# Kernel tuning notes

Hardware: AMD Instinct MI355X
Metric: run time of the kernel (lower is better)

The kernel has to match this reference:

```python
import jax, jax.numpy as jnp
import numpy as np

NUM_LAYERS = 3
CODEBOOK_SIZE = 2048
EMBED_DIM = 256
B, T = 16, 2048


def setup_inputs() -> dict:
    key = jax.random.key(0)
    k1, k2 = jax.random.split(key)
    h = jax.random.normal(k1, (B, T, EMBED_DIM), dtype=jnp.float32)
    codebooks = jax.random.normal(k2, (NUM_LAYERS, CODEBOOK_SIZE, EMBED_DIM), dtype=jnp.float32)
    return {"h": h, "codebooks": codebooks}


def reference(h, codebooks):
    """Residual VQ: 3 sequential layers of nearest-codeword quantization.
    h: (B, T, D); codebooks: (L, K, D).
    Returns (quantized_total (B,T,D), indices (L, B, T)).
    """
    residual = h
    quantized_total = jnp.zeros_like(h)
    all_indices = []
    for l in range(codebooks.shape[0]):
        W = codebooks[l]  # (K, D)
        # ||r - w||^2 = ||r||^2 - 2 r.w + ||w||^2 ; same argmin as the naive broadcast form.
        r_sq = jnp.sum(residual * residual, axis=-1, keepdims=True)         # (B, T, 1)
        w_sq = jnp.sum(W * W, axis=-1)                                      # (K,)
        cross = jnp.einsum('btd,kd->btk', residual, W)                      # (B, T, K)
        dists = r_sq - 2.0 * cross + w_sq                                   # (B, T, K)
        indices = jnp.argmin(dists, axis=-1)                                # (B, T)
        all_indices.append(indices)
        quant = W[indices]                                                  # gather -> (B, T, D)
        quantized_total = quantized_total + quant
        residual = residual - quant
    return quantized_total, jnp.stack(all_indices, axis=0)
```

## Files before the change

kernel.cpp:

```cpp
#include <hip/hip_runtime.h>
#include <math.h>

#define NUM_LAYERS 3
#define KCB 2048
#define DIM 256
#define NROWS 32768
#define NQ (NROWS * DIM)

#define F_BYTES (3u * 128u * 16384u)

#define BSH_OFF  0
#define BV_OFF   131072
#define BI_OFF   132096
#define BIDX_OFF 133120
#define SMEM_BYTES 133632

typedef _Float16 half8 __attribute__((ext_vector_type(8)));
typedef float   f32x4 __attribute__((ext_vector_type(4)));

__global__ void rvq_wsq(const float* __restrict__ cb, float* __restrict__ wsq)
{
    int tid = blockIdx.x * 256 + threadIdx.x;
    const float* p = cb + (size_t)tid * DIM;
    float s = 0.f;
    #pragma unroll
    for (int u = 0; u < 64; ++u) {
        float4 v = *(const float4*)(p + u * 4);
        s = fmaf(v.x, v.x, s); s = fmaf(v.y, v.y, s);
        s = fmaf(v.z, v.z, s); s = fmaf(v.w, v.w, s);
    }
    wsq[tid] = s;
}

__global__ void rvq_repack(const float* __restrict__ cb, unsigned short* __restrict__ F)
{
    int b = blockIdx.x;
    int layer = b >> 10;
    int rem   = b & 1023;
    int tn    = rem >> 3;
    int kb    = rem & 7;
    int lane  = threadIdx.x;

    int cw = tn * 16 + (lane & 15);
    int k0 = kb * 32 + (lane >> 4) * 8;
    const float* src = cb + ((size_t)(layer * KCB + cw)) * DIM + k0;
    float4 x0 = *(const float4*)(src);
    float4 x1 = *(const float4*)(src + 4);
    float v[8] = {x0.x, x0.y, x0.z, x0.w, x1.x, x1.y, x1.z, x1.w};

    half8 hi, lo;
    #pragma unroll
    for (int j = 0; j < 8; ++j) {
        _Float16 h = (_Float16)v[j];
        hi[j] = h;
        lo[j] = (_Float16)(v[j] - (float)h);
    }
    size_t base = ((size_t)b) * 1024;
    *(half8*)(F + base + lane * 8)        = hi;
    *(half8*)(F + base + 512 + lane * 8)  = lo;
}

__device__ __forceinline__ void stage_chunk(const char* Fb, char* Bsh,
                                            int c, int buf, int wv, int lane)
{
    #pragma unroll
    for (int i = 0; i < 8; ++i) {
        int s = wv * 8 + i;
        int tm = s >> 5;
        int off = (s & 31) * 1024;
        const char* g = Fb + (size_t)tm * 1048576 + (size_t)c * 32768 + off + (size_t)lane * 16;
        char* lp = Bsh + (size_t)buf * 65536 + (size_t)tm * 32768 + off + (size_t)lane * 16;
        __builtin_amdgcn_global_load_lds(
            (const __attribute__((address_space(1))) unsigned int*)g,
            (__attribute__((address_space(3))) unsigned int*)lp, 16, 0, 0);
    }
}

__global__ __launch_bounds__(512, 2)
void rvq_main(const float* __restrict__ h,
              const float* __restrict__ cb,
              const unsigned short* __restrict__ F,
              const float* __restrict__ wsq,
              float* __restrict__ out)
{
    extern __shared__ char smem[];
    char*  Bsh     = smem + BSH_OFF;
    float* bV_sh   = (float*)(smem + BV_OFF);
    int*   bI_sh   = (int*)  (smem + BI_OFF);
    int*   bidx_sh = (int*)  (smem + BIDX_OFF);

    const int t      = threadIdx.x;
    const int lane   = t & 63;
    const int wv     = t >> 6;
    const int team   = wv & 1;
    const int rgroup = wv >> 1;
    const int rowB   = blockIdx.x * 128;
    const int row0w  = rowB + rgroup * 32;
    const int arow   = lane & 15;
    const int aq     = lane >> 4;

    half8 ahi[2][8], alo[2][8];
    float s2[2];
    #pragma unroll
    for (int mi = 0; mi < 2; ++mi) {
        s2[mi] = 0.f;
        #pragma unroll
        for (int kb = 0; kb < 8; ++kb) {
            const float* p = h + (size_t)(row0w + mi * 16 + arow) * DIM + kb * 32 + aq * 8;
            float4 x0 = *(const float4*)(p);
            float4 x1 = *(const float4*)(p + 4);
            float v[8] = {x0.x, x0.y, x0.z, x0.w, x1.x, x1.y, x1.z, x1.w};
            #pragma unroll
            for (int j = 0; j < 8; ++j) {
                _Float16 hv = (_Float16)v[j];
                ahi[mi][kb][j] = hv;
                alo[mi][kb][j] = (_Float16)(v[j] - (float)hv);
                s2[mi] = fmaf(v[j], v[j], s2[mi]);
            }
        }
    }

    stage_chunk((const char*)F, Bsh, 0, 0, wv, lane);

    for (int l = 0; l < NUM_LAYERS; ++l) {
        const float* __restrict__ Wl  = cb + (size_t)l * KCB * DIM;
        const float* __restrict__ wql = wsq + l * KCB;
        const char*  Fb = (const char*)F + (size_t)l * 2097152;

        float a0 = s2[0], a1 = s2[1];
        a0 += __shfl_xor(a0, 16); a0 += __shfl_xor(a0, 32);
        a1 += __shfl_xor(a1, 16); a1 += __shfl_xor(a1, 32);
        float rsqC[2][4];
        #pragma unroll
        for (int i = 0; i < 4; ++i) {
            rsqC[0][i] = __shfl(a0, aq * 4 + i, 16);
            rsqC[1][i] = __shfl(a1, aq * 4 + i, 16);
        }

        float bestV[2][4];
        int   bestI[2][4];
        #pragma unroll
        for (int mi = 0; mi < 2; ++mi)
            #pragma unroll
            for (int i = 0; i < 4; ++i) { bestV[mi][i] = INFINITY; bestI[mi][i] = 0; }

        __syncthreads();

        for (int c = 0; c < 32; ++c) {
            const int cur = c & 1;
            if (c + 1 < 32) stage_chunk(Fb, Bsh, c + 1, 1 - cur, wv, lane);

            #pragma unroll
            for (int ti = 0; ti < 2; ++ti) {
                const char* base = Bsh + (size_t)cur * 65536 + (size_t)team * 32768 + (size_t)ti * 16384;
                f32x4 acc[2][2];
                const f32x4 z = {0.f, 0.f, 0.f, 0.f};
                acc[0][0] = z; acc[0][1] = z; acc[1][0] = z; acc[1][1] = z;
                #pragma unroll
                for (int kb = 0; kb < 8; ++kb) {
                    half8 bhi = *(const half8*)(base + kb * 2048 + lane * 16);
                    half8 blo = *(const half8*)(base + kb * 2048 + 1024 + lane * 16);
                    const int p = kb & 1;
                    acc[0][p] = __builtin_amdgcn_mfma_f32_16x16x32_f16(ahi[0][kb], bhi, acc[0][p], 0, 0, 0);
                    acc[1][p] = __builtin_amdgcn_mfma_f32_16x16x32_f16(ahi[1][kb], bhi, acc[1][p], 0, 0, 0);
                    acc[0][p] = __builtin_amdgcn_mfma_f32_16x16x32_f16(alo[0][kb], bhi, acc[0][p], 0, 0, 0);
                    acc[1][p] = __builtin_amdgcn_mfma_f32_16x16x32_f16(alo[1][kb], bhi, acc[1][p], 0, 0, 0);
                    acc[0][p] = __builtin_amdgcn_mfma_f32_16x16x32_f16(ahi[0][kb], blo, acc[0][p], 0, 0, 0);
                    acc[1][p] = __builtin_amdgcn_mfma_f32_16x16x32_f16(ahi[1][kb], blo, acc[1][p], 0, 0, 0);
                }
                const int col = team * 1024 + (c * 2 + ti) * 16 + arow;
                const float wq = wql[col];
                #pragma unroll
                for (int mi = 0; mi < 2; ++mi)
                    #pragma unroll
                    for (int i = 0; i < 4; ++i) {
                        float cc = acc[mi][0][i] + acc[mi][1][i];
                        float dist = (rsqC[mi][i] - 2.f * cc) + wq;
                        if (dist < bestV[mi][i]) { bestV[mi][i] = dist; bestI[mi][i] = col; }
                    }
            }
            __syncthreads();
        }

        #pragma unroll
        for (int mi = 0; mi < 2; ++mi)
            #pragma unroll
            for (int i = 0; i < 4; ++i) {
                float bv = bestV[mi][i]; int bi = bestI[mi][i];
                #pragma unroll
                for (int s = 8; s; s >>= 1) {
                    float ov = __shfl_xor(bv, s, 16);
                    int   oi = __shfl_xor(bi, s, 16);
                    if (ov < bv || (ov == bv && oi < bi)) { bv = ov; bi = oi; }
                }
                bestV[mi][i] = bv; bestI[mi][i] = bi;
            }
        if (arow == 0) {
            #pragma unroll
            for (int mi = 0; mi < 2; ++mi)
                #pragma unroll
                for (int i = 0; i < 4; ++i) {
                    bV_sh[wv * 32 + mi * 16 + aq * 4 + i] = bestV[mi][i];
                    bI_sh[wv * 32 + mi * 16 + aq * 4 + i] = bestI[mi][i];
                }
        }
        __syncthreads();

        if (t < 128) {
            int rg = t >> 5, rl = t & 31;
            float v0 = bV_sh[(rg * 2 + 0) * 32 + rl]; int i0 = bI_sh[(rg * 2 + 0) * 32 + rl];
            float v1 = bV_sh[(rg * 2 + 1) * 32 + rl]; int i1 = bI_sh[(rg * 2 + 1) * 32 + rl];
            int bi = (v1 < v0 || (v1 == v0 && i1 < i0)) ? i1 : i0;
            bidx_sh[t] = bi;
            out[NQ + (size_t)l * NROWS + rowB + t] = (float)bi;
        }
        if (l < NUM_LAYERS - 1)
            stage_chunk(Fb + 2097152, Bsh, 0, 0, wv, lane);
        __syncthreads();

        if (l < NUM_LAYERS - 1) {
            #pragma unroll
            for (int mi = 0; mi < 2; ++mi) {
                const int bi = bidx_sh[rgroup * 32 + mi * 16 + arow];
                const float* wrow = Wl + (size_t)bi * DIM;
                float ns = 0.f;
                #pragma unroll
                for (int kb = 0; kb < 8; ++kb) {
                    const float* wp = wrow + kb * 32 + aq * 8;
                    float4 w0 = *(const float4*)(wp);
                    float4 w1 = *(const float4*)(wp + 4);
                    float wv8[8] = {w0.x, w0.y, w0.z, w0.w, w1.x, w1.y, w1.z, w1.w};
                    #pragma unroll
                    for (int j = 0; j < 8; ++j) {
                        float r = ((float)ahi[mi][kb][j] + (float)alo[mi][kb][j]) - wv8[j];
                        _Float16 hv = (_Float16)r;
                        ahi[mi][kb][j] = hv;
                        alo[mi][kb][j] = (_Float16)(r - (float)hv);
                        ns = fmaf(r, r, ns);
                    }
                }
                s2[mi] = ns;
            }
        } else {
            const int mi  = team;
            const int row = row0w + mi * 16 + arow;
            const int bi  = bidx_sh[rgroup * 32 + mi * 16 + arow];
            const float* wrow = Wl + (size_t)bi * DIM;
            #pragma unroll
            for (int kb = 0; kb < 8; ++kb) {
                const float* wp = wrow + kb * 32 + aq * 8;
                const float* hp = h + (size_t)row * DIM + kb * 32 + aq * 8;
                float4 w0 = *(const float4*)(wp);
                float4 w1 = *(const float4*)(wp + 4);
                float4 h0 = *(const float4*)(hp);
                float4 h1 = *(const float4*)(hp + 4);
                float wv8[8] = {w0.x, w0.y, w0.z, w0.w, w1.x, w1.y, w1.z, w1.w};
                float hv8[8] = {h0.x, h0.y, h0.z, h0.w, h1.x, h1.y, h1.z, h1.w};
                float o[8];
                #pragma unroll
                for (int j = 0; j < 8; ++j) {
                    float r = ((float)ahi[mi][kb][j] + (float)alo[mi][kb][j]) - wv8[j];
                    o[j] = hv8[j] - r;
                }
                float* op = out + (size_t)row * DIM + kb * 32 + aq * 8;
                *(float4*)(op)     = make_float4(o[0], o[1], o[2], o[3]);
                *(float4*)(op + 4) = make_float4(o[4], o[5], o[6], o[7]);
            }
        }
    }
}

extern "C" void kernel_launch(void* const* d_in, const int* in_sizes, int n_in,
                              void* d_out, int out_size, void* d_ws, size_t ws_size,
                              hipStream_t stream) {
    const float* h  = (const float*)d_in[0];
    const float* cb = (const float*)d_in[1];
    float* out = (float*)d_out;
    unsigned short* F = (unsigned short*)d_ws;
    float* wsq = (float*)((char*)d_ws + F_BYTES);

    hipFuncSetAttribute((const void*)rvq_main,
                        hipFuncAttributeMaxDynamicSharedMemorySize, SMEM_BYTES);

    rvq_wsq   <<<dim3(24),   dim3(256), 0, stream>>>(cb, wsq);
    rvq_repack<<<dim3(3072), dim3(64),  0, stream>>>(cb, F);
    rvq_main  <<<dim3(NROWS / 128), dim3(512), SMEM_BYTES, stream>>>(h, cb, F, wsq, out);
}
```

Baseline: 413.4 us.

## Switch distance GEMM from 16x16x32 to 32x32x16 MFMA tiles

Each wave now computes one 32-row by 32-codeword tile with the 32x32x16 f16 MFMA, replacing two 16x16 tiles per row half. The codebook repack layout, A-operand register layout, residual-norm distribution (now staged through shared memory), argmin reduction and epilogue indexing are all reorganized to match the new fragment layout. The larger tile is meant to raise MFMA efficiency and reduce LDS B-fragment reads per FLOP. The cost is 16-entry accumulators and best-value arrays, which raise register pressure and may hurt occupancy.

Result: slower. 473.8 us (+14.6%).

```diff
diff --git a/kernel.cpp b/kernel.cpp
--- a/kernel.cpp
+++ b/kernel.cpp
@@ -7,16 +7,17 @@
 #define NROWS 32768
 #define NQ (NROWS * DIM)
 
-#define F_BYTES (3u * 128u * 16384u)
+#define F_BYTES (3u * 2097152u)
 
 #define BSH_OFF  0
-#define BV_OFF   131072
-#define BI_OFF   132096
-#define BIDX_OFF 133120
-#define SMEM_BYTES 133632
+#define RSQ_OFF  131072
+#define BV_OFF   131584
+#define BI_OFF   132608
+#define BIDX_OFF 133632
+#define SMEM_BYTES 134144
 
 typedef _Float16 half8 __attribute__((ext_vector_type(8)));
-typedef float   f32x4 __attribute__((ext_vector_type(4)));
+typedef float   f32x16 __attribute__((ext_vector_type(16)));
 
 __global__ void rvq_wsq(const float* __restrict__ cb, float* __restrict__ wsq)
 {
@@ -37,12 +38,13 @@
     int b = blockIdx.x;
     int layer = b >> 10;
     int rem   = b & 1023;
-    int tn    = rem >> 3;
-    int kb    = rem & 7;
+    int team  = rem >> 9;
+    int c     = (rem >> 4) & 31;
+    int ks    = rem & 15;
     int lane  = threadIdx.x;
 
-    int cw = tn * 16 + (lane & 15);
-    int k0 = kb * 32 + (lane >> 4) * 8;
+    int cw = team * 1024 + c * 32 + (lane & 31);
+    int k0 = ks * 16 + (lane >> 5) * 8;
     const float* src = cb + ((size_t)(layer * KCB + cw)) * DIM + k0;
     float4 x0 = *(const float4*)(src);
     float4 x1 = *(const float4*)(src + 4);
@@ -85,6 +87,7 @@
 {
     extern __shared__ char smem[];
     char*  Bsh     = smem + BSH_OFF;
+    float* rsq_sh  = (float*)(smem + RSQ_OFF);
     float* bV_sh   = (float*)(smem + BV_OFF);
     int*   bI_sh   = (int*)  (smem + BI_OFF);
     int*   bidx_sh = (int*)  (smem + BIDX_OFF);
@@ -96,26 +99,24 @@
     const int rgroup = wv >> 1;
     const int rowB   = blockIdx.x * 128;
     const int row0w  = rowB + rgroup * 32;
-    const int arow   = lane & 15;
-    const int aq     = lane >> 4;
-
-    half8 ahi[2][8], alo[2][8];
-    float s2[2];
-    #pragma unroll
-    for (int mi = 0; mi < 2; ++mi) {
-        s2[mi] = 0.f;
-        #pragma unroll
-        for (int kb = 0; kb < 8; ++kb) {
-            const float* p = h + (size_t)(row0w + mi * 16 + arow) * DIM + kb * 32 + aq * 8;
-            float4 x0 = *(const float4*)(p);
-            float4 x1 = *(const float4*)(p + 4);
+    const int ln     = lane & 31;
+    const int lh     = lane >> 5;
+
+    half8 ahi[16], alo[16];
+    float s2 = 0.f;
+    {
+        const float* rp = h + (size_t)(row0w + ln) * DIM + lh * 8;
+        #pragma unroll
+        for (int ks = 0; ks < 16; ++ks) {
+            float4 x0 = *(const float4*)(rp + ks * 16);
+            float4 x1 = *(const float4*)(rp + ks * 16 + 4);
             float v[8] = {x0.x, x0.y, x0.z, x0.w, x1.x, x1.y, x1.z, x1.w};
             #pragma unroll
             for (int j = 0; j < 8; ++j) {
                 _Float16 hv = (_Float16)v[j];
-                ahi[mi][kb][j] = hv;
-                alo[mi][kb][j] = (_Float16)(v[j] - (float)hv);
-                s2[mi] = fmaf(v[j], v[j], s2[mi]);
+                ahi[ks][j] = hv;
+                alo[ks][j] = (_Float16)(v[j] - (float)hv);
+                s2 = fmaf(v[j], v[j], s2);
             }
         }
     }
@@ -127,82 +128,69 @@
         const float* __restrict__ wql = wsq + l * KCB;
         const char*  Fb = (const char*)F + (size_t)l * 2097152;
 
-        float a0 = s2[0], a1 = s2[1];
-        a0 += __shfl_xor(a0, 16); a0 += __shfl_xor(a0, 32);
-        a1 += __shfl_xor(a1, 16); a1 += __shfl_xor(a1, 32);
-        float rsqC[2][4];
-        #pragma unroll
-        for (int i = 0; i < 4; ++i) {
-            rsqC[0][i] = __shfl(a0, aq * 4 + i, 16);
-            rsqC[1][i] = __shfl(a1, aq * 4 + i, 16);
-        }
-
-        float bestV[2][4];
-        int   bestI[2][4];
-        #pragma unroll
-        for (int mi = 0; mi < 2; ++mi)
-            #pragma unroll
-            for (int i = 0; i < 4; ++i) { bestV[mi][i] = INFINITY; bestI[mi][i] = 0; }
-
+        float rs = s2 + __shfl_xor(s2, 32);
+        if (team == 0 && lh == 0) rsq_sh[rgroup * 32 + ln] = rs;
         __syncthreads();
+
+        float rsqR[16];
+        #pragma unroll
+        for (int r = 0; r < 16; ++r)
+            rsqR[r] = rsq_sh[rgroup * 32 + (r & 3) + 8 * (r >> 2) + 4 * lh];
+
+        float bestV[16];
+        int   bestI[16];
+        #pragma unroll
+        for (int r = 0; r < 16; ++r) { bestV[r] = INFINITY; bestI[r] = 0; }
 
         for (int c = 0; c < 32; ++c) {
             const int cur = c & 1;
             if (c + 1 < 32) stage_chunk(Fb, Bsh, c + 1, 1 - cur, wv, lane);
 
-            #pragma unroll
-            for (int ti = 0; ti < 2; ++ti) {
-                const char* base = Bsh + (size_t)cur * 65536 + (size_t)team * 32768 + (size_t)ti * 16384;
-                f32x4 acc[2][2];
-                const f32x4 z = {0.f, 0.f, 0.f, 0.f};
-                acc[0][0] = z; acc[0][1] = z; acc[1][0] = z; acc[1][1] = z;
-                #pragma unroll
-                for (int kb = 0; kb < 8; ++kb) {
-                    half8 bhi = *(const half8*)(base + kb * 2048 + lane * 16);
-                    half8 blo = *(const half8*)(base + kb * 2048 + 1024 + lane * 16);
-                    const int p = kb & 1;
-                    acc[0][p] = __builtin_amdgcn_mfma_f32_16x16x32_f16(ahi[0][kb], bhi, acc[0][p], 0, 0, 0);
-                    acc[1][p] = __builtin_amdgcn_mfma_f32_16x16x32_f16(ahi[1][kb], bhi, acc[1][p], 0, 0, 0);
-                    acc[0][p] = __builtin_amdgcn_mfma_f32_16x16x32_f16(alo[0][kb], bhi, acc[0][p], 0, 0, 0);
-                    acc[1][p] = __builtin_amdgcn_mfma_f32_16x16x32_f16(alo[1][kb], bhi, acc[1][p], 0, 0, 0);
-                    acc[0][p] = __builtin_amdgcn_mfma_f32_16x16x32_f16(ahi[0][kb], blo, acc[0][p], 0, 0, 0);
-                    acc[1][p] = __builtin_amdgcn_mfma_f32_16x16x32_f16(ahi[1][kb], blo, acc[1][p], 0, 0, 0);
+            const char* base = Bsh + (size_t)cur * 65536 + (size_t)team * 32768;
+            f32x16 acc0 = {}, acc1 = {};
+            #pragma unroll
+            for (int ks = 0; ks < 16; ++ks) {
+                half8 bhi = *(const half8*)(base + ks * 2048 + lane * 16);
+                half8 blo = *(const half8*)(base + ks * 2048 + 1024 + lane * 16);
+                if (ks & 1) {
+                    acc1 = __builtin_amdgcn_mfma_f32_32x32x16_f16(ahi[ks], bhi, acc1, 0, 0, 0);
+                    acc1 = __builtin_amdgcn_mfma_f32_32x32x16_f16(alo[ks], bhi, acc1, 0, 0, 0);
+                    acc1 = __builtin_amdgcn_mfma_f32_32x32x16_f16(ahi[ks], blo, acc1, 0, 0, 0);
+                } else {
+                    acc0 = __builtin_amdgcn_mfma_f32_32x32x16_f16(ahi[ks], bhi, acc0, 0, 0, 0);
+                    acc0 = __builtin_amdgcn_mfma_f32_32x32x16_f16(alo[ks], bhi, acc0, 0, 0, 0);
+                    acc0 = __builtin_amdgcn_mfma_f32_32x32x16_f16(ahi[ks], blo, acc0, 0, 0, 0);
                 }
-                const int col = team * 1024 + (c * 2 + ti) * 16 + arow;
-                const float wq = wql[col];
-                #pragma unroll
-                for (int mi = 0; mi < 2; ++mi)
-                    #pragma unroll
-                    for (int i = 0; i < 4; ++i) {
-                        float cc = acc[mi][0][i] + acc[mi][1][i];
-                        float dist = (rsqC[mi][i] - 2.f * cc) + wq;
-                        if (dist < bestV[mi][i]) { bestV[mi][i] = dist; bestI[mi][i] = col; }
-                    }
+            }
+            const int col = team * 1024 + c * 32 + ln;
+            const float wq = wql[col];
+            #pragma unroll
+            for (int r = 0; r < 16; ++r) {
+                float cc = acc0[r] + acc1[r];
+                float dist = (rsqR[r] - 2.f * cc) + wq;
+                if (dist < bestV[r]) { bestV[r] = dist; bestI[r] = col; }
             }
             __syncthreads();
         }
 
         #pragma unroll
-        for (int mi = 0; mi < 2; ++mi)
-            #pragma unroll
-            for (int i = 0; i < 4; ++i) {
-                float bv = bestV[mi][i]; int bi = bestI[mi][i];
-                #pragma unroll
-                for (int s = 8; s; s >>= 1) {
-                    float ov = __shfl_xor(bv, s, 16);
-                    int   oi = __shfl_xor(bi, s, 16);
-                    if (ov < bv || (ov == bv && oi < bi)) { bv = ov; bi = oi; }
-                }
-                bestV[mi][i] = bv; bestI[mi][i] = bi;
-            }
-        if (arow == 0) {
-            #pragma unroll
-            for (int mi = 0; mi < 2; ++mi)
-                #pragma unroll
-                for (int i = 0; i < 4; ++i) {
-                    bV_sh[wv * 32 + mi * 16 + aq * 4 + i] = bestV[mi][i];
-                    bI_sh[wv * 32 + mi * 16 + aq * 4 + i] = bestI[mi][i];
-                }
+        for (int r = 0; r < 16; ++r) {
+            float bv = bestV[r]; int bi = bestI[r];
+            #pragma unroll
+            for (int s = 16; s; s >>= 1) {
+                float ov = __shfl_xor(bv, s);
+                int   oi = __shfl_xor(bi, s);
+                if (ov < bv || (ov == bv && oi < bi)) { bv = ov; bi = oi; }
+            }
+            bestV[r] = bv; bestI[r] = bi;
+        }
+        if (ln == 0) {
+            #pragma unroll
+            for (int r = 0; r < 16; ++r) {
+                int row = (r & 3) + 8 * (r >> 2) + 4 * lh;
+                bV_sh[wv * 32 + row] = bestV[r];
+                bI_sh[wv * 32 + row] = bestI[r];
+            }
         }
         __syncthreads();
 
@@ -219,52 +207,47 @@
         __syncthreads();
 
         if (l < NUM_LAYERS - 1) {
-            #pragma unroll
-            for (int mi = 0; mi < 2; ++mi) {
-                const int bi = bidx_sh[rgroup * 32 + mi * 16 + arow];
-                const float* wrow = Wl + (size_t)bi * DIM;
-                float ns = 0.f;
+            const int bi = bidx_sh[rgroup * 32 + ln];
+            const float* wrow = Wl + (size_t)bi * DIM + lh * 8;
+            float ns = 0.f;
+            #pragma unroll
+            for (int ks = 0; ks < 16; ++ks) {
+                float4 w0 = *(const float4*)(wrow + ks * 16);
+                float4 w1 = *(const float4*)(wrow + ks * 16 + 4);
+                float wv8[8] = {w0.x, w0.y, w0.z, w0.w, w1.x, w1.y, w1.z, w1.w};
                 #pragma unroll
-                for (int kb = 0; kb < 8; ++kb) {
-                    const float* wp = wrow + kb * 32 + aq * 8;
-                    float4 w0 = *(const float4*)(wp);
-                    float4 w1 = *(const float4*)(wp + 4);
-                    float wv8[8] = {w0.x, w0.y, w0.z, w0.w, w1.x, w1.y, w1.z, w1.w};
-                    #pragma unroll
-                    for (int j = 0; j < 8; ++j) {
-                        float r = ((float)ahi[mi][kb][j] + (float)alo[mi][kb][j]) - wv8[j];
-                        _Float16 hv = (_Float16)r;
-                        ahi[mi][kb][j] = hv;
-                        alo[mi][kb][j] = (_Float16)(r - (float)hv);
-                        ns = fmaf(r, r, ns);
-                    }
+                for (int j = 0; j < 8; ++j) {
+                    float r = ((float)ahi[ks][j] + (float)alo[ks][j]) - wv8[j];
+                    _Float16 hv = (_Float16)r;
+                    ahi[ks][j] = hv;
+                    alo[ks][j] = (_Float16)(r - (float)hv);
+                    ns = fmaf(r, r, ns);
                 }
-                s2[mi] = ns;
-            }
+            }
+            s2 = ns;
         } else {
-            const int mi  = team;
-            const int row = row0w + mi * 16 + arow;
-            const int bi  = bidx_sh[rgroup * 32 + mi * 16 + arow];
-            const float* wrow = Wl + (size_t)bi * DIM;
-            #pragma unroll
-            for (int kb = 0; kb < 8; ++kb) {
-                const float* wp = wrow + kb * 32 + aq * 8;
-                const float* hp = h + (size_t)row * DIM + kb * 32 + aq * 8;
-                float4 w0 = *(const float4*)(wp);
-                float4 w1 = *(const float4*)(wp + 4);
-                float4 h0 = *(const float4*)(hp);
-                float4 h1 = *(const float4*)(hp + 4);
+            const int row = row0w + ln;
+            const int bi  = bidx_sh[rgroup * 32 + ln];
+            const float* wrow = Wl + (size_t)bi * DIM + lh * 8;
+            const float* hp   = h + (size_t)row * DIM + lh * 8;
+            float* op         = out + (size_t)row * DIM + lh * 8;
+            #pragma unroll
+            for (int ksi = 0; ksi < 8; ++ksi) {
+                const int ks = team * 8 + ksi;
+                float4 w0 = *(const float4*)(wrow + ks * 16);
+                float4 w1 = *(const float4*)(wrow + ks * 16 + 4);
+                float4 h0 = *(const float4*)(hp + ks * 16);
+                float4 h1 = *(const float4*)(hp + ks * 16 + 4);
                 float wv8[8] = {w0.x, w0.y, w0.z, w0.w, w1.x, w1.y, w1.z, w1.w};
                 float hv8[8] = {h0.x, h0.y, h0.z, h0.w, h1.x, h1.y, h1.z, h1.w};
                 float o[8];
                 #pragma unroll
                 for (int j = 0; j < 8; ++j) {
-                    float r = ((float)ahi[mi][kb][j] + (float)alo[mi][kb][j]) - wv8[j];
+                    float r = ((float)ahi[ks][j] + (float)alo[ks][j]) - wv8[j];
                     o[j] = hv8[j] - r;
                 }
-                float* op = out + (size_t)row * DIM + kb * 32 + aq * 8;
-                *(float4*)(op)     = make_float4(o[0], o[1], o[2], o[3]);
-                *(float4*)(op + 4) = make_float4(o[4], o[5], o[6], o[7]);
+                *(float4*)(op + ks * 16)     = make_float4(o[0], o[1], o[2], o[3]);
+                *(float4*)(op + ks * 16 + 4) = make_float4(o[4], o[5], o[6], o[7]);
             }
         }
     }
```

## Split the K dimension across wave pairs and exchange partial dot products via LDS

Applied to the files above, without the earlier changes.

Each wave pair now splits the 256-wide reduction dimension in half instead of splitting codewords. Each wave keeps only half of the A fragments in registers, which halves per-thread fp16 register storage. Both waves compute partials for two 16-codeword tiles and swap one partial through a new LDS exchange buffer. Staging chunks shrink to 32 codewords with a 64-iteration loop, and LDS use drops from about 133 KB to about 102 KB. In exchange it adds LDS traffic and a partial-sum exchange per chunk, with a barrier on every iteration.

Result: faster. 374.5 us (-9.4%).

```diff
diff --git a/kernel.cpp b/kernel.cpp
--- a/kernel.cpp
+++ b/kernel.cpp
@@ -10,10 +10,12 @@
 #define F_BYTES (3u * 128u * 16384u)
 
 #define BSH_OFF  0
-#define BV_OFF   131072
-#define BI_OFF   132096
-#define BIDX_OFF 133120
-#define SMEM_BYTES 133632
+#define XCH_OFF  65536
+#define RSQP_OFF 98304
+#define BV_OFF   99328
+#define BI_OFF   100352
+#define BIDX_OFF 101376
+#define SMEM_BYTES 101888
 
 typedef _Float16 half8 __attribute__((ext_vector_type(8)));
 typedef float   f32x4 __attribute__((ext_vector_type(4)));
@@ -60,20 +62,47 @@
     *(half8*)(F + base + 512 + lane * 8)  = lo;
 }
 
-__device__ __forceinline__ void stage_chunk(const char* Fb, char* Bsh,
-                                            int c, int buf, int wv, int lane)
-{
-    #pragma unroll
-    for (int i = 0; i < 8; ++i) {
-        int s = wv * 8 + i;
-        int tm = s >> 5;
-        int off = (s & 31) * 1024;
-        const char* g = Fb + (size_t)tm * 1048576 + (size_t)c * 32768 + off + (size_t)lane * 16;
-        char* lp = Bsh + (size_t)buf * 65536 + (size_t)tm * 32768 + off + (size_t)lane * 16;
+__device__ __forceinline__ void stage_chunk32(const char* Fb, char* dst, int c, int t)
+{
+    const char* g = Fb + (size_t)c * 32768;
+    #pragma unroll
+    for (int i = 0; i < 4; ++i) {
+        int off = (i * 512 + t) * 16;
         __builtin_amdgcn_global_load_lds(
-            (const __attribute__((address_space(1))) unsigned int*)g,
-            (__attribute__((address_space(3))) unsigned int*)lp, 16, 0, 0);
-    }
+            (const __attribute__((address_space(1))) unsigned int*)(g + off),
+            (__attribute__((address_space(3))) unsigned int*)(dst + off), 16, 0, 0);
+    }
+}
+
+__device__ __forceinline__ void tile_partial(
+    const char* tbase, const half8 (&ahi)[2][4], const half8 (&alo)[2][4],
+    int kt, int lane, f32x4 (&po)[2])
+{
+    const f32x4 z = {0.f, 0.f, 0.f, 0.f};
+    f32x4 a00 = z, a01 = z, a10 = z, a11 = z;
+    #pragma unroll
+    for (int kq = 0; kq < 4; ++kq) {
+        const int kb = kt * 4 + kq;
+        half8 bhi = *(const half8*)(tbase + kb * 2048 + lane * 16);
+        half8 blo = *(const half8*)(tbase + kb * 2048 + 1024 + lane * 16);
+        if (kq & 1) {
+            a01 = __builtin_amdgcn_mfma_f32_16x16x32_f16(ahi[0][kq], bhi, a01, 0, 0, 0);
+            a11 = __builtin_amdgcn_mfma_f32_16x16x32_f16(ahi[1][kq], bhi, a11, 0, 0, 0);
+            a01 = __builtin_amdgcn_mfma_f32_16x16x32_f16(alo[0][kq], bhi, a01, 0, 0, 0);
+            a11 = __builtin_amdgcn_mfma_f32_16x16x32_f16(alo[1][kq], bhi, a11, 0, 0, 0);
+            a01 = __builtin_amdgcn_mfma_f32_16x16x32_f16(ahi[0][kq], blo, a01, 0, 0, 0);
+            a11 = __builtin_amdgcn_mfma_f32_16x16x32_f16(ahi[1][kq], blo, a11, 0, 0, 0);
+        } else {
+            a00 = __builtin_amdgcn_mfma_f32_16x16x32_f16(ahi[0][kq], bhi, a00, 0, 0, 0);
+            a10 = __builtin_amdgcn_mfma_f32_16x16x32_f16(ahi[1][kq], bhi, a10, 0, 0, 0);
+            a00 = __builtin_amdgcn_mfma_f32_16x16x32_f16(alo[0][kq], bhi, a00, 0, 0, 0);
+            a10 = __builtin_amdgcn_mfma_f32_16x16x32_f16(alo[1][kq], bhi, a10, 0, 0, 0);
+            a00 = __builtin_amdgcn_mfma_f32_16x16x32_f16(ahi[0][kq], blo, a00, 0, 0, 0);
+            a10 = __builtin_amdgcn_mfma_f32_16x16x32_f16(ahi[1][kq], blo, a10, 0, 0, 0);
+        }
+    }
+    #pragma unroll
+    for (int i = 0; i < 4; ++i) { po[0][i] = a00[i] + a01[i]; po[1][i] = a10[i] + a11[i]; }
 }
 
 __global__ __launch_bounds__(512, 2)
@@ -85,42 +114,44 @@
 {
     extern __shared__ char smem[];
     char*  Bsh     = smem + BSH_OFF;
+    char*  Xch     = smem + XCH_OFF;
+    float* rsqp    = (float*)(smem + RSQP_OFF);
     float* bV_sh   = (float*)(smem + BV_OFF);
     int*   bI_sh   = (int*)  (smem + BI_OFF);
     int*   bidx_sh = (int*)  (smem + BIDX_OFF);
 
-    const int t      = threadIdx.x;
-    const int lane   = t & 63;
-    const int wv     = t >> 6;
-    const int team   = wv & 1;
-    const int rgroup = wv >> 1;
-    const int rowB   = blockIdx.x * 128;
-    const int row0w  = rowB + rgroup * 32;
-    const int arow   = lane & 15;
-    const int aq     = lane >> 4;
-
-    half8 ahi[2][8], alo[2][8];
+    const int t     = threadIdx.x;
+    const int lane  = t & 63;
+    const int wv    = t >> 6;
+    const int kt    = wv & 1;
+    const int rg    = wv >> 1;
+    const int rowB  = blockIdx.x * 128;
+    const int row0w = rowB + rg * 32;
+    const int arow  = lane & 15;
+    const int aq    = lane >> 4;
+
+    half8 ahi[2][4], alo[2][4];
     float s2[2];
     #pragma unroll
     for (int mi = 0; mi < 2; ++mi) {
         s2[mi] = 0.f;
         #pragma unroll
-        for (int kb = 0; kb < 8; ++kb) {
-            const float* p = h + (size_t)(row0w + mi * 16 + arow) * DIM + kb * 32 + aq * 8;
+        for (int kq = 0; kq < 4; ++kq) {
+            const float* p = h + (size_t)(row0w + mi * 16 + arow) * DIM + (kt * 4 + kq) * 32 + aq * 8;
             float4 x0 = *(const float4*)(p);
             float4 x1 = *(const float4*)(p + 4);
             float v[8] = {x0.x, x0.y, x0.z, x0.w, x1.x, x1.y, x1.z, x1.w};
             #pragma unroll
             for (int j = 0; j < 8; ++j) {
                 _Float16 hv = (_Float16)v[j];
-                ahi[mi][kb][j] = hv;
-                alo[mi][kb][j] = (_Float16)(v[j] - (float)hv);
+                ahi[mi][kq][j] = hv;
+                alo[mi][kq][j] = (_Float16)(v[j] - (float)hv);
                 s2[mi] = fmaf(v[j], v[j], s2[mi]);
             }
         }
     }
 
-    stage_chunk((const char*)F, Bsh, 0, 0, wv, lane);
+    stage_chunk32((const char*)F, Bsh, 0, t);
 
     for (int l = 0; l < NUM_LAYERS; ++l) {
         const float* __restrict__ Wl  = cb + (size_t)l * KCB * DIM;
@@ -130,12 +161,20 @@
         float a0 = s2[0], a1 = s2[1];
         a0 += __shfl_xor(a0, 16); a0 += __shfl_xor(a0, 32);
         a1 += __shfl_xor(a1, 16); a1 += __shfl_xor(a1, 32);
+        if (aq == 0) {
+            rsqp[kt * 128 + rg * 32 + arow]      = a0;
+            rsqp[kt * 128 + rg * 32 + 16 + arow] = a1;
+        }
+        __syncthreads();
+
         float rsqC[2][4];
         #pragma unroll
-        for (int i = 0; i < 4; ++i) {
-            rsqC[0][i] = __shfl(a0, aq * 4 + i, 16);
-            rsqC[1][i] = __shfl(a1, aq * 4 + i, 16);
-        }
+        for (int mi = 0; mi < 2; ++mi)
+            #pragma unroll
+            for (int i = 0; i < 4; ++i) {
+                int row = rg * 32 + mi * 16 + aq * 4 + i;
+                rsqC[mi][i] = rsqp[row] + rsqp[128 + row];
+            }
 
         float bestV[2][4];
         int   bestI[2][4];
@@ -144,42 +183,38 @@
             #pragma unroll
             for (int i = 0; i < 4; ++i) { bestV[mi][i] = INFINITY; bestI[mi][i] = 0; }
 
-        __syncthreads();
-
-        for (int c = 0; c < 32; ++c) {
+        for (int c = 0; c < 64; ++c) {
             const int cur = c & 1;
-            if (c + 1 < 32) stage_chunk(Fb, Bsh, c + 1, 1 - cur, wv, lane);
-
-            #pragma unroll
-            for (int ti = 0; ti < 2; ++ti) {
-                const char* base = Bsh + (size_t)cur * 65536 + (size_t)team * 32768 + (size_t)ti * 16384;
-                f32x4 acc[2][2];
-                const f32x4 z = {0.f, 0.f, 0.f, 0.f};
-                acc[0][0] = z; acc[0][1] = z; acc[1][0] = z; acc[1][1] = z;
-                #pragma unroll
-                for (int kb = 0; kb < 8; ++kb) {
-                    half8 bhi = *(const half8*)(base + kb * 2048 + lane * 16);
-                    half8 blo = *(const half8*)(base + kb * 2048 + 1024 + lane * 16);
-                    const int p = kb & 1;
-                    acc[0][p] = __builtin_amdgcn_mfma_f32_16x16x32_f16(ahi[0][kb], bhi, acc[0][p], 0, 0, 0);
-                    acc[1][p] = __builtin_amdgcn_mfma_f32_16x16x32_f16(ahi[1][kb], bhi, acc[1][p], 0, 0, 0);
-                    acc[0][p] = __builtin_amdgcn_mfma_f32_16x16x32_f16(alo[0][kb], bhi, acc[0][p], 0, 0, 0);
-                    acc[1][p] = __builtin_amdgcn_mfma_f32_16x16x32_f16(alo[1][kb], bhi, acc[1][p], 0, 0, 0);
-                    acc[0][p] = __builtin_amdgcn_mfma_f32_16x16x32_f16(ahi[0][kb], blo, acc[0][p], 0, 0, 0);
-                    acc[1][p] = __builtin_amdgcn_mfma_f32_16x16x32_f16(ahi[1][kb], blo, acc[1][p], 0, 0, 0);
-                }
-                const int col = team * 1024 + (c * 2 + ti) * 16 + arow;
-                const float wq = wql[col];
-                #pragma unroll
-                for (int mi = 0; mi < 2; ++mi)
-                    #pragma unroll
-                    for (int i = 0; i < 4; ++i) {
-                        float cc = acc[mi][0][i] + acc[mi][1][i];
-                        float dist = (rsqC[mi][i] - 2.f * cc) + wq;
-                        if (dist < bestV[mi][i]) { bestV[mi][i] = dist; bestI[mi][i] = col; }
-                    }
-            }
+            if (c + 1 < 64) stage_chunk32(Fb, Bsh + (size_t)(1 - cur) * 32768, c + 1, t);
+            const char* bb = Bsh + (size_t)cur * 32768;
+
+            {
+                f32x4 pn[2];
+                tile_partial(bb + (size_t)(1 - kt) * 16384, ahi, alo, kt, lane, pn);
+                char* xw = Xch + (size_t)cur * 16384 + rg * 4096 + kt * 2048;
+                *(f32x4*)(xw + lane * 16)        = pn[0];
+                *(f32x4*)(xw + 1024 + lane * 16) = pn[1];
+            }
+            f32x4 po[2];
+            tile_partial(bb + (size_t)kt * 16384, ahi, alo, kt, lane, po);
+
             __syncthreads();
+
+            const char* xr = Xch + (size_t)cur * 16384 + rg * 4096 + (1 - kt) * 2048;
+            f32x4 pp0 = *(const f32x4*)(xr + lane * 16);
+            f32x4 pp1 = *(const f32x4*)(xr + 1024 + lane * 16);
+
+            const int col = c * 32 + kt * 16 + arow;
+            const float wq = wql[col];
+            #pragma unroll
+            for (int i = 0; i < 4; ++i) {
+                float c0 = po[0][i] + pp0[i];
+                float d0 = (rsqC[0][i] - 2.f * c0) + wq;
+                if (d0 < bestV[0][i]) { bestV[0][i] = d0; bestI[0][i] = col; }
+                float c1 = po[1][i] + pp1[i];
+                float d1 = (rsqC[1][i] - 2.f * c1) + wq;
+                if (d1 < bestV[1][i]) { bestV[1][i] = d1; bestI[1][i] = col; }
+            }
         }
 
         #pragma unroll
@@ -207,64 +242,67 @@
         __syncthreads();
 
         if (t < 128) {
-            int rg = t >> 5, rl = t & 31;
-            float v0 = bV_sh[(rg * 2 + 0) * 32 + rl]; int i0 = bI_sh[(rg * 2 + 0) * 32 + rl];
-            float v1 = bV_sh[(rg * 2 + 1) * 32 + rl]; int i1 = bI_sh[(rg * 2 + 1) * 32 + rl];
+            int rgi = t >> 5, rl = t & 31;
+            float v0 = bV_sh[(rgi * 2 + 0) * 32 + rl]; int i0 = bI_sh[(rgi * 2 + 0) * 32 + rl];
+            float v1 = bV_sh[(rgi * 2 + 1) * 32 + rl]; int i1 = bI_sh[(rgi * 2 + 1) * 32 + rl];
             int bi = (v1 < v0 || (v1 == v0 && i1 < i0)) ? i1 : i0;
             bidx_sh[t] = bi;
             out[NQ + (size_t)l * NROWS + rowB + t] = (float)bi;
         }
         if (l < NUM_LAYERS - 1)
-            stage_chunk(Fb + 2097152, Bsh, 0, 0, wv, lane);
+            stage_chunk32(Fb + 2097152, Bsh, 0, t);
         __syncthreads();
 
         if (l < NUM_LAYERS - 1) {
             #pragma unroll
             for (int mi = 0; mi < 2; ++mi) {
-                const int bi = bidx_sh[rgroup * 32 + mi * 16 + arow];
+                const int bi = bidx_sh[rg * 32 + mi * 16 + arow];
                 const float* wrow = Wl + (size_t)bi * DIM;
                 float ns = 0.f;
                 #pragma unroll
-                for (int kb = 0; kb < 8; ++kb) {
-                    const float* wp = wrow + kb * 32 + aq * 8;
+                for (int kq = 0; kq < 4; ++kq) {
+                    const float* wp = wrow + (kt * 4 + kq) * 32 + aq * 8;
                     float4 w0 = *(const float4*)(wp);
                     float4 w1 = *(const float4*)(wp + 4);
                     float wv8[8] = {w0.x, w0.y, w0.z, w0.w, w1.x, w1.y, w1.z, w1.w};
                     #pragma unroll
                     for (int j = 0; j < 8; ++j) {
-                        float r = ((float)ahi[mi][kb][j] + (float)alo[mi][kb][j]) - wv8[j];
+                        float r = ((float)ahi[mi][kq][j] + (float)alo[mi][kq][j]) - wv8[j];
                         _Float16 hv = (_Float16)r;
-                        ahi[mi][kb][j] = hv;
-                        alo[mi][kb][j] = (_Float16)(r - (float)hv);
+                        ahi[mi][kq][j] = hv;
+                        alo[mi][kq][j] = (_Float16)(r - (float)hv);
                         ns = fmaf(r, r, ns);
                     }
                 }
                 s2[mi] = ns;
             }
         } else {
-            const int mi  = team;
-            const int row = row0w + mi * 16 + arow;
-            const int bi  = bidx_sh[rgroup * 32 + mi * 16 + arow];
-            const float* wrow = Wl + (size_t)bi * DIM;
-            #pragma unroll
-            for (int kb = 0; kb < 8; ++kb) {
-                const float* wp = wrow + kb * 32 + aq * 8;
-                const float* hp = h + (size_t)row * DIM + kb * 32 + aq * 8;
-                float4 w0 = *(const float4*)(wp);
-                float4 w1 = *(const float4*)(wp + 4);
-                float4 h0 = *(const float4*)(hp);
-                float4 h1 = *(const float4*)(hp + 4);
-                float wv8[8] = {w0.x, w0.y, w0.z, w0.w, w1.x, w1.y, w1.z, w1.w};
-                float hv8[8] = {h0.x, h0.y, h0.z, h0.w, h1.x, h1.y, h1.z, h1.w};
-                float o[8];
+            #pragma unroll
+            for (int mi = 0; mi < 2; ++mi) {
+                const int row = row0w + mi * 16 + arow;
+                const int bi  = bidx_sh[rg * 32 + mi * 16 + arow];
+                const float* wrow = Wl + (size_t)bi * DIM;
                 #pragma unroll
-                for (int j = 0; j < 8; ++j) {
-                    float r = ((float)ahi[mi][kb][j] + (float)alo[mi][kb][j]) - wv8[j];
-                    o[j] = hv8[j] - r;
+                for (int kq = 0; kq < 4; ++kq) {
+                    const int ko = (kt * 4 + kq) * 32 + aq * 8;
+                    const float* wp = wrow + ko;
+                    const float* hp = h + (size_t)row * DIM + ko;
+                    float4 w0 = *(const float4*)(wp);
+                    float4 w1 = *(const float4*)(wp + 4);
+                    float4 h0 = *(const float4*)(hp);
+                    float4 h1 = *(const float4*)(hp + 4);
+                    float wv8[8] = {w0.x, w0.y, w0.z, w0.w, w1.x, w1.y, w1.z, w1.w};
+                    float hv8[8] = {h0.x, h0.y, h0.z, h0.w, h1.x, h1.y, h1.z, h1.w};
+                    float o[8];
+                    #pragma unroll
+                    for (int j = 0; j < 8; ++j) {
+                        float r = ((float)ahi[mi][kq][j] + (float)alo[mi][kq][j]) - wv8[j];
+                        o[j] = hv8[j] - r;
+                    }
+                    float* op = out + (size_t)row * DIM + ko;
+                    *(float4*)(op)     = make_float4(o[0], o[1], o[2], o[3]);
+                    *(float4*)(op + 4) = make_float4(o[4], o[5], o[6], o[7]);
                 }
-                float* op = out + (size_t)row * DIM + kb * 32 + aq * 8;
-                *(float4*)(op)     = make_float4(o[0], o[1], o[2], o[3]);
-                *(float4*)(op + 4) = make_float4(o[4], o[5], o[6], o[7]);
             }
         }
     }
```
